# Optimization experiments

Measured on AMD Instinct MI355X. Metric: run time of the kernel, lower is better.

Reference implementation:

```python
import jax, jax.numpy as jnp
import numpy as np

N, E, D_IN, D_H, D_OUT = 50000, 800000, 128, 128, 40
EPS = 1e-5


def setup_inputs() -> dict:
    key = jax.random.key(0)
    ks = jax.random.split(key, 12)
    x = jax.random.normal(ks[0], (N, D_IN), dtype=jnp.float32)
    edge_index = jax.random.randint(ks[1], (2, E), 0, N, dtype=jnp.int32)
    s = 1.0 / np.sqrt(D_H)
    return {
        "x": x,
        "edge_index": edge_index,
        "W1": jax.random.normal(ks[2], (D_IN, D_H), jnp.float32) * s,
        "b1": jnp.zeros((D_H,), jnp.float32),
        "W2": jax.random.normal(ks[3], (D_H, D_H), jnp.float32) * s,
        "b2": jnp.zeros((D_H,), jnp.float32),
        "g1": jnp.ones((D_H,), jnp.float32),
        "be1": jnp.zeros((D_H,), jnp.float32),
        "g2": jnp.ones((D_H,), jnp.float32),
        "be2": jnp.zeros((D_H,), jnp.float32),
        "g3": jnp.ones((D_H,), jnp.float32),
        "be3": jnp.zeros((D_H,), jnp.float32),
        "Wm": jax.random.normal(ks[4], (D_H, D_OUT), jnp.float32) * s,
        "bm": jnp.zeros((D_OUT,), jnp.float32),
    }


def _gcn_conv(x, W, b, src, dst, dinv):
    # GCNConv: x' = D^{-1/2}(A+I)D^{-1/2} (x W) + b
    xw = x @ W                                   # [N, H]
    coef = dinv[src] * dinv[dst]                 # [E]
    agg = jax.ops.segment_sum(xw[src] * coef[:, None], dst, num_segments=x.shape[0])
    agg = agg + xw * (dinv * dinv)[:, None]      # self-loop term
    return agg + b


def _bn(x, g, b):
    # BatchNorm1d in training mode: biased batch statistics over nodes
    m = jnp.mean(x, axis=0)
    v = jnp.var(x, axis=0)
    return g * (x - m) * jax.lax.rsqrt(v + EPS) + b


def reference(x, edge_index, W1, b1, W2, b2, g1, be1, g2, be2, g3, be3, Wm, bm):
    src, dst = edge_index[0], edge_index[1]
    # degree with self-loops (GCN symmetric normalization, computed on dst/col)
    deg = 1.0 + jax.ops.segment_sum(jnp.ones((E,), jnp.float32), dst, num_segments=N)
    dinv = jax.lax.rsqrt(deg)
    h = _gcn_conv(x, W1, b1, src, dst, dinv)
    h = jax.nn.relu(_bn(h, g1, be1))            # dropout is identity in eval
    h = _gcn_conv(h, W2, b2, src, dst, dinv)
    h = jax.nn.relu(_bn(h, g2, be2))
    h = _bn(h, g3, be3)
    h = h @ Wm + bm
    return jax.nn.log_softmax(h, axis=1)
```

## Files before the change

### kernel.cpp

```cpp
#include <hip/hip_runtime.h>
#include <hip/hip_fp16.h>
#include <math.h>

#define BN_EPS 1e-5f
#define CAP 128
#define NSTAT 200

typedef __attribute__((ext_vector_type(8))) short short8;
typedef __attribute__((ext_vector_type(4))) float floatx4;

__device__ inline unsigned short f2bf(float f) {
    union { float f; unsigned u; } x; x.f = f;
    unsigned r = x.u + 0x7fff + ((x.u >> 16) & 1);
    return (unsigned short)(r >> 16);
}
__device__ inline float bf2f(unsigned short h) {
    union { float f; unsigned u; } x; x.u = ((unsigned)h) << 16; return x.f;
}
__device__ inline void bn_sc_sh(float sum, float sumsq, float g, float be, float invN,
                                float& sc, float& sh) {
    float mean = sum * invN;
    float var = sumsq * invN - mean * mean;
    sc = g * rsqrtf(var + BN_EPS);
    sh = be - mean * sc;
}

__device__ inline void pack_one(int idx, const float* W1, const float* W2, const float* Wm,
                                unsigned short* p1, unsigned short* p2, unsigned short* pm) {
    const float* W;
    unsigned short* pack;
    int f, l = idx & 63, t, n, stride, ncols;
    if (idx < 2048) {
        W = W1; pack = p1; f = idx >> 6; t = f >> 3; n = (f & 7) * 16 + (l & 15);
        stride = 128; ncols = 128;
    } else if (idx < 4096) {
        W = W2; pack = p2; f = (idx - 2048) >> 6; t = f >> 3; n = (f & 7) * 16 + (l & 15);
        stride = 128; ncols = 128;
    } else {
        W = Wm; pack = pm; f = (idx - 4096) >> 6; t = f / 3; n = (f % 3) * 16 + (l & 15);
        stride = 40; ncols = 40;
    }
    int q = l >> 4;
    unsigned short* pp = pack + f * 1024 + l * 16;
#pragma unroll
    for (int j = 0; j < 8; ++j) {
        int k = t * 32 + q * 8 + j;
        float v = (n < ncols) ? W[k * stride + n] : 0.f;
        unsigned short hi = f2bf(v);
        float lo = v - bf2f(hi);
        pp[j] = hi;
        pp[8 + j] = f2bf(lo);
    }
}

__global__ __launch_bounds__(256) void k_zero_pack(const float* W1, const float* W2,
                                                   const float* Wm, unsigned short* p1,
                                                   unsigned short* p2, unsigned short* pm,
                                                   int* fillc, float* stats, int N) {
    int gtid = blockIdx.x * 256 + threadIdx.x;
    int gsz = gridDim.x * 256;
    for (int i = gtid; i < N; i += gsz) fillc[i] = 0;
    for (int i = gtid; i < 768; i += gsz) stats[i] = 0.f;
    for (int i = gtid; i < 4864; i += gsz) pack_one(i, W1, W2, Wm, p1, p2, pm);
}

__global__ void k_fill(const int* __restrict__ src, const int* __restrict__ dst, int E,
                       int* __restrict__ fillc, unsigned short* __restrict__ col16) {
    int g = blockIdx.x & 7;
    int rank = blockIdx.x >> 3;
    int stride = (gridDim.x >> 3) * 256;
    for (int e = rank * 256 + threadIdx.x; e < E; e += stride) {
        int d = dst[e];
        if ((d & 7) != g) continue;
        int r = atomicAdd(&fillc[d], 1);
        if (r < CAP) col16[(size_t)d * CAP + r] = (unsigned short)src[e];
    }
}

__device__ inline void load_row8(const float* arow, int kbase, float av[8]) {
    float4 a0 = *(const float4*)(arow + kbase);
    float4 a1 = *(const float4*)(arow + kbase + 4);
    av[0] = a0.x; av[1] = a0.y; av[2] = a0.z; av[3] = a0.w;
    av[4] = a1.x; av[5] = a1.y; av[6] = a1.z; av[7] = a1.w;
}
__device__ inline void load_row8(const __half* arow, int kbase, float av[8]) {
    float4 raw = *(const float4*)(arow + kbase);
    const __half2* h = (const __half2*)&raw;
#pragma unroll
    for (int i = 0; i < 4; ++i) {
        float2 f = __half22float2(h[i]);
        av[2 * i] = f.x;
        av[2 * i + 1] = f.y;
    }
}

template <typename T, bool FUSE_BN>
__device__ void gemm_phase(const T* __restrict__ A, const unsigned short* __restrict__ packW,
                           const float* __restrict__ sums, const float* __restrict__ g,
                           const float* __restrict__ be, float invN,
                           const int* __restrict__ fillc, __half* __restrict__ C16, int M,
                           int waveId, int nwaves, int lane) {
    int row = lane & 15, quad = lane >> 4;
    for (int m0 = waveId * 16; m0 < M; m0 += nwaves * 16) {
        floatx4 acc[8];
#pragma unroll
        for (int nt = 0; nt < 8; ++nt) acc[nt] = (floatx4){0.f, 0.f, 0.f, 0.f};
        int mr = m0 + row;
        if (mr >= M) mr = M - 1;
        const T* arow = A + (size_t)mr * 128;
#pragma unroll
        for (int t = 0; t < 4; ++t) {
            int kbase = t * 32 + quad * 8;
            float av[8];
            load_row8(arow, kbase, av);
            if (FUSE_BN) {
#pragma unroll
                for (int j = 0; j < 8; ++j) {
                    int c = kbase + j;
                    float sc, sh;
                    bn_sc_sh(sums[c], sums[128 + c], g[c], be[c], invN, sc, sh);
                    av[j] = fmaxf(av[j] * sc + sh, 0.f);
                }
            }
            short8 ah, al;
#pragma unroll
            for (int j = 0; j < 8; ++j) {
                unsigned short hi = f2bf(av[j]);
                ah[j] = (short)hi;
                al[j] = (short)f2bf(av[j] - bf2f(hi));
            }
            const unsigned short* wp = packW + (size_t)(t * 8) * 1024 + lane * 16;
#pragma unroll
            for (int nt = 0; nt < 8; ++nt) {
                short8 wh = *(const short8*)wp;
                short8 wl = *(const short8*)(wp + 8);
                wp += 1024;
                acc[nt] = __builtin_amdgcn_mfma_f32_16x16x32_bf16(ah, wh, acc[nt], 0, 0, 0);
                acc[nt] = __builtin_amdgcn_mfma_f32_16x16x32_bf16(al, wh, acc[nt], 0, 0, 0);
                acc[nt] = __builtin_amdgcn_mfma_f32_16x16x32_bf16(ah, wl, acc[nt], 0, 0, 0);
            }
        }
        float d[4];
#pragma unroll
        for (int r = 0; r < 4; ++r) {
            int m = m0 + quad * 4 + r;
            d[r] = (m < M) ? rsqrtf(1.f + (float)fillc[m]) : 0.f;
        }
#pragma unroll
        for (int nt = 0; nt < 8; ++nt) {
#pragma unroll
            for (int r = 0; r < 4; ++r) {
                int m = m0 + quad * 4 + r;
                if (m < M)
                    C16[(size_t)m * 128 + nt * 16 + row] = __float2half_rn(acc[nt][r] * d[r]);
            }
        }
    }
}

__global__ __launch_bounds__(256) void k_gemm1(const float* A, const unsigned short* pW,
                                               const int* fillc, __half* C, int M) {
    gemm_phase<float, false>(A, pW, nullptr, nullptr, nullptr, 0.f, fillc, C, M,
                             blockIdx.x * 4 + (threadIdx.x >> 6), gridDim.x * 4,
                             threadIdx.x & 63);
}
__global__ __launch_bounds__(256) void k_gemm2(const __half* A, const unsigned short* pW,
                                               const float* sums, const float* g,
                                               const float* be, float invN, const int* fillc,
                                               __half* C, int M) {
    gemm_phase<__half, true>(A, pW, sums, g, be, invN, fillc, C, M,
                             blockIdx.x * 4 + (threadIdx.x >> 6), gridDim.x * 4,
                             threadIdx.x & 63);
}

__global__ __launch_bounds__(256) void k_gath(const __half* __restrict__ y16,
                                              const int* __restrict__ fillc,
                                              const unsigned short* __restrict__ col16,
                                              const float* __restrict__ bias,
                                              __half* __restrict__ out, int N) {
    int wv = threadIdx.x >> 6;
    int lane = threadIdx.x & 63;
    int n = blockIdx.x * 4 + wv;
    if (n >= N) return;
    int sub = lane >> 4;
    int c8 = (lane & 15) << 3;

    float acc[8];
#pragma unroll
    for (int i = 0; i < 8; ++i) acc[i] = 0.f;

    int degraw = fillc[n];
    int deg = min(degraw, CAP);
    const unsigned short* cb = col16 + (size_t)n * CAP;
    for (int jb = 0; jb < deg; jb += 64) {
        int cnt = min(64, deg - jb);
        int idx = (lane < cnt) ? (int)cb[jb + lane] : 0;
        int jj = 0;
        for (; jj + 16 <= cnt; jj += 16) {
            int s0 = __shfl(idx, jj + sub, 64);
            int s1 = __shfl(idx, jj + 4 + sub, 64);
            int s2 = __shfl(idx, jj + 8 + sub, 64);
            int s3 = __shfl(idx, jj + 12 + sub, 64);
            float4 r0 = *(const float4*)(y16 + (size_t)s0 * 128 + c8);
            float4 r1 = *(const float4*)(y16 + (size_t)s1 * 128 + c8);
            float4 r2 = *(const float4*)(y16 + (size_t)s2 * 128 + c8);
            float4 r3 = *(const float4*)(y16 + (size_t)s3 * 128 + c8);
            const __half2* h0 = (const __half2*)&r0;
            const __half2* h1 = (const __half2*)&r1;
            const __half2* h2 = (const __half2*)&r2;
            const __half2* h3 = (const __half2*)&r3;
#pragma unroll
            for (int i = 0; i < 4; ++i) {
                float2 f0 = __half22float2(h0[i]);
                float2 f1 = __half22float2(h1[i]);
                float2 f2 = __half22float2(h2[i]);
                float2 f3 = __half22float2(h3[i]);
                acc[2 * i] += (f0.x + f1.x) + (f2.x + f3.x);
                acc[2 * i + 1] += (f0.y + f1.y) + (f2.y + f3.y);
            }
        }
        for (; jj < cnt; jj += 4) {
            int jt = jj + sub;
            bool valid = jt < cnt;
            int s = __shfl(idx, valid ? jt : 0, 64);
            float4 r = *(const float4*)(y16 + (size_t)s * 128 + c8);
            if (valid) {
                const __half2* hh = (const __half2*)&r;
#pragma unroll
                for (int i = 0; i < 4; ++i) {
                    float2 f = __half22float2(hh[i]);
                    acc[2 * i] += f.x;
                    acc[2 * i + 1] += f.y;
                }
            }
        }
    }
#pragma unroll
    for (int i = 0; i < 8; ++i) {
        acc[i] += __shfl_xor(acc[i], 16, 64);
        acc[i] += __shfl_xor(acc[i], 32, 64);
    }
    if (sub == 0) {
        float dn = rsqrtf(1.f + (float)degraw);
        float4 selfraw = *(const float4*)(y16 + (size_t)n * 128 + c8);
        const __half2* sh = (const __half2*)&selfraw;
        float4 b0 = *(const float4*)(bias + c8);
        float4 b1 = *(const float4*)(bias + c8 + 4);
        float bb[8] = {b0.x, b0.y, b0.z, b0.w, b1.x, b1.y, b1.z, b1.w};
        __half2 o[4];
#pragma unroll
        for (int i = 0; i < 4; ++i) {
            float2 sf = __half22float2(sh[i]);
            float vx = dn * (acc[2 * i] + sf.x) + bb[2 * i];
            float vy = dn * (acc[2 * i + 1] + sf.y) + bb[2 * i + 1];
            o[i] = __float22half2_rn(make_float2(vx, vy));
        }
        *(float4*)(out + (size_t)n * 128 + c8) = *(float4*)o;
    }
}

template <bool TRANSFORM>
__global__ __launch_bounds__(256) void k_stats_s(const __half2* __restrict__ h, int N,
                                                 const float* __restrict__ sums2,
                                                 const float* __restrict__ g2,
                                                 const float* __restrict__ be2, float invN,
                                                 float* __restrict__ statsOut) {
    __shared__ float ls[4][256];
    int tid = threadIdx.x, bid = blockIdx.x;
    int cp = tid & 63, rg = tid >> 6;
    float scx = 1.f, shx = 0.f, scy = 1.f, shy = 0.f;
    if (TRANSFORM) {
        int c = cp * 2;
        bn_sc_sh(sums2[c], sums2[128 + c], g2[c], be2[c], invN, scx, shx);
        bn_sc_sh(sums2[c + 1], sums2[128 + c + 1], g2[c + 1], be2[c + 1], invN, scy, shy);
    }
    float sx = 0.f, sy = 0.f, s2x = 0.f, s2y = 0.f;
    for (int r = bid * 4 + rg; r < N; r += NSTAT * 4) {
        float2 v = __half22float2(h[(size_t)r * 64 + cp]);
        if (TRANSFORM) {
            v.x = fmaxf(v.x * scx + shx, 0.f);
            v.y = fmaxf(v.y * scy + shy, 0.f);
        }
        sx += v.x; sy += v.y;
        s2x += v.x * v.x; s2y += v.y * v.y;
    }
    ls[0][tid] = sx; ls[1][tid] = sy; ls[2][tid] = s2x; ls[3][tid] = s2y;
    __syncthreads();
    if (tid < 64) {
        float a0 = ls[0][tid] + ls[0][tid + 64] + ls[0][tid + 128] + ls[0][tid + 192];
        float a1 = ls[1][tid] + ls[1][tid + 64] + ls[1][tid + 128] + ls[1][tid + 192];
        float a2 = ls[2][tid] + ls[2][tid + 64] + ls[2][tid + 128] + ls[2][tid + 192];
        float a3 = ls[3][tid] + ls[3][tid + 64] + ls[3][tid + 128] + ls[3][tid + 192];
        atomicAdd(&statsOut[2 * tid], a0);
        atomicAdd(&statsOut[2 * tid + 1], a1);
        atomicAdd(&statsOut[128 + 2 * tid], a2);
        atomicAdd(&statsOut[128 + 2 * tid + 1], a3);
    }
}

__global__ __launch_bounds__(256) void k_final_s(const __half* __restrict__ h,
                                                 const float* __restrict__ sums2,
                                                 const float* __restrict__ g2,
                                                 const float* __restrict__ be2,
                                                 const float* __restrict__ sums3,
                                                 const float* __restrict__ g3,
                                                 const float* __restrict__ be3, float invN,
                                                 const unsigned short* __restrict__ packWm,
                                                 const float* __restrict__ bm,
                                                 float* __restrict__ out, int N) {
    int lane = threadIdx.x & 63;
    int wv = threadIdx.x >> 6;
    int m0 = (blockIdx.x * 4 + wv) * 16;
    if (m0 >= N) return;
    int row = lane & 15, quad = lane >> 4;

    floatx4 acc[3];
#pragma unroll
    for (int nt = 0; nt < 3; ++nt) acc[nt] = (floatx4){0.f, 0.f, 0.f, 0.f};

    int mr = m0 + row;
    if (mr >= N) mr = N - 1;
    const __half* arow = h + (size_t)mr * 128;
#pragma unroll
    for (int t = 0; t < 4; ++t) {
        int kbase = t * 32 + quad * 8;
        float av[8];
        load_row8(arow, kbase, av);
#pragma unroll
        for (int j = 0; j < 8; ++j) {
            int c = kbase + j;
            float sc2, sh2, sc3, sh3;
            bn_sc_sh(sums2[c], sums2[128 + c], g2[c], be2[c], invN, sc2, sh2);
            bn_sc_sh(sums3[c], sums3[128 + c], g3[c], be3[c], invN, sc3, sh3);
            av[j] = fmaxf(av[j] * sc2 + sh2, 0.f) * sc3 + sh3;
        }
        short8 ah, al;
#pragma unroll
        for (int j = 0; j < 8; ++j) {
            unsigned short hi = f2bf(av[j]);
            ah[j] = (short)hi;
            al[j] = (short)f2bf(av[j] - bf2f(hi));
        }
        const unsigned short* wp = packWm + (size_t)(t * 3) * 1024 + lane * 16;
#pragma unroll
        for (int nt = 0; nt < 3; ++nt) {
            short8 wh = *(const short8*)wp;
            short8 wl = *(const short8*)(wp + 8);
            wp += 1024;
            acc[nt] = __builtin_amdgcn_mfma_f32_16x16x32_bf16(ah, wh, acc[nt], 0, 0, 0);
            acc[nt] = __builtin_amdgcn_mfma_f32_16x16x32_bf16(al, wh, acc[nt], 0, 0, 0);
            acc[nt] = __builtin_amdgcn_mfma_f32_16x16x32_bf16(ah, wl, acc[nt], 0, 0, 0);
        }
    }
    float bb[3];
#pragma unroll
    for (int nt = 0; nt < 3; ++nt) {
        int col = nt * 16 + row;
        bb[nt] = (col < 40) ? bm[col] : 0.f;
    }
    bool val2 = (row < 8);
#pragma unroll
    for (int r = 0; r < 4; ++r) {
        int m = m0 + quad * 4 + r;
        float v0 = acc[0][r] + bb[0];
        float v1 = acc[1][r] + bb[1];
        float v2 = acc[2][r] + bb[2];
        float mx = fmaxf(v0, v1);
        if (val2) mx = fmaxf(mx, v2);
#pragma unroll
        for (int off = 1; off <= 8; off <<= 1) mx = fmaxf(mx, __shfl_xor(mx, off, 64));
        float s = expf(v0 - mx) + expf(v1 - mx) + (val2 ? expf(v2 - mx) : 0.f);
#pragma unroll
        for (int off = 1; off <= 8; off <<= 1) s += __shfl_xor(s, off, 64);
        float lse = mx + logf(s);
        if (m < N) {
            out[(size_t)m * 40 + row] = v0 - lse;
            out[(size_t)m * 40 + 16 + row] = v1 - lse;
            if (val2) out[(size_t)m * 40 + 32 + row] = v2 - lse;
        }
    }
}

extern "C" void kernel_launch(void* const* d_in, const int* in_sizes, int n_in,
                              void* d_out, int out_size, void* d_ws, size_t ws_size,
                              hipStream_t stream) {
    const float* x   = (const float*)d_in[0];
    const int*   ei  = (const int*)d_in[1];
    const float* W1  = (const float*)d_in[2];
    const float* b1  = (const float*)d_in[3];
    const float* W2  = (const float*)d_in[4];
    const float* b2  = (const float*)d_in[5];
    const float* g1  = (const float*)d_in[6];
    const float* be1 = (const float*)d_in[7];
    const float* g2  = (const float*)d_in[8];
    const float* be2 = (const float*)d_in[9];
    const float* g3  = (const float*)d_in[10];
    const float* be3 = (const float*)d_in[11];
    const float* Wm  = (const float*)d_in[12];
    const float* bm  = (const float*)d_in[13];
    float* out = (float*)d_out;

    int N = in_sizes[0] / 128;
    int E = in_sizes[1] / 2;
    float invN = 1.0f / (float)N;

    char* ws = (char*)d_ws;
    size_t off = 0;
    auto alloc = [&](size_t bytes) -> void* {
        void* p = ws + off;
        off += (bytes + 255) & ~(size_t)255;
        return p;
    };
    int*   fillc    = (int*)alloc((size_t)N * 4);
    float* statsAll = (float*)alloc(768 * 4);
    unsigned short* col16 = (unsigned short*)alloc((size_t)N * CAP * 2);
    unsigned short* pW1 = (unsigned short*)alloc(32768 * 2);
    unsigned short* pW2 = (unsigned short*)alloc(32768 * 2);
    unsigned short* pWm = (unsigned short*)alloc(12288 * 2);
    __half* y16 = (__half*)alloc((size_t)N * 128 * 2);
    __half* h16 = (__half*)alloc((size_t)N * 128 * 2);
    (void)ws_size; (void)n_in; (void)out_size;

    int gb = (N + 63) / 64;
    int gatherb = (N + 3) / 4;

    k_zero_pack<<<64, 256, 0, stream>>>(W1, W2, Wm, pW1, pW2, pWm, fillc, statsAll, N);
    k_fill<<<1024, 256, 0, stream>>>(ei, ei + E, E, fillc, col16);

    k_gemm1<<<gb, 256, 0, stream>>>(x, pW1, fillc, y16, N);
    k_gath<<<gatherb, 256, 0, stream>>>(y16, fillc, col16, b1, h16, N);
    k_stats_s<false><<<NSTAT, 256, 0, stream>>>((const __half2*)h16, N, nullptr, nullptr,
                                                nullptr, invN, statsAll);
    k_gemm2<<<gb, 256, 0, stream>>>(h16, pW2, statsAll, g1, be1, invN, fillc, y16, N);
    k_gath<<<gatherb, 256, 0, stream>>>(y16, fillc, col16, b2, h16, N);
    k_stats_s<false><<<NSTAT, 256, 0, stream>>>((const __half2*)h16, N, nullptr, nullptr,
                                                nullptr, invN, statsAll + 256);
    k_stats_s<true><<<NSTAT, 256, 0, stream>>>((const __half2*)h16, N, statsAll + 256, g2, be2,
                                               invN, statsAll + 512);
    k_final_s<<<gb, 256, 0, stream>>>(h16, statsAll + 256, g2, be2, statsAll + 512, g3, be3,
                                      invN, pWm, bm, out, N);
}
```

Measured before the change: 340.7 us.

## Merge pipeline stages into cooperative persistent kernels with grid syncs

Replaces the chain of separate launches (zero/pack, fill, gather, stats, final) with three cooperative persistent kernels that use grid.sync between phases, keeping the two GEMMs as normal launches. The aim is to remove per-kernel launch gaps and tail effects across the many small stages. In exchange, gathers now use a grid-stride loop over a fixed grid, which may reduce latency hiding, and each grid sync has its own cost. A fallback to the old launch sequence remains for when cooperative launch fails.

```diff
diff --git a/kernel.cpp b/kernel.cpp
--- a/kernel.cpp
+++ b/kernel.cpp
@@ -1,6 +1,9 @@
 #include <hip/hip_runtime.h>
 #include <hip/hip_fp16.h>
+#include <hip/hip_cooperative_groups.h>
 #include <math.h>
+
+namespace cg = cooperative_groups;
 
 #define BN_EPS 1e-5f
 #define CAP 128
@@ -53,30 +56,6 @@
     }
 }
 
-__global__ __launch_bounds__(256) void k_zero_pack(const float* W1, const float* W2,
-                                                   const float* Wm, unsigned short* p1,
-                                                   unsigned short* p2, unsigned short* pm,
-                                                   int* fillc, float* stats, int N) {
-    int gtid = blockIdx.x * 256 + threadIdx.x;
-    int gsz = gridDim.x * 256;
-    for (int i = gtid; i < N; i += gsz) fillc[i] = 0;
-    for (int i = gtid; i < 768; i += gsz) stats[i] = 0.f;
-    for (int i = gtid; i < 4864; i += gsz) pack_one(i, W1, W2, Wm, p1, p2, pm);
-}
-
-__global__ void k_fill(const int* __restrict__ src, const int* __restrict__ dst, int E,
-                       int* __restrict__ fillc, unsigned short* __restrict__ col16) {
-    int g = blockIdx.x & 7;
-    int rank = blockIdx.x >> 3;
-    int stride = (gridDim.x >> 3) * 256;
-    for (int e = rank * 256 + threadIdx.x; e < E; e += stride) {
-        int d = dst[e];
-        if ((d & 7) != g) continue;
-        int r = atomicAdd(&fillc[d], 1);
-        if (r < CAP) col16[(size_t)d * CAP + r] = (unsigned short)src[e];
-    }
-}
-
 __device__ inline void load_row8(const float* arow, int kbase, float av[8]) {
     float4 a0 = *(const float4*)(arow + kbase);
     float4 a1 = *(const float4*)(arow + kbase + 4);
@@ -173,120 +152,115 @@
                              threadIdx.x & 63);
 }
 
-__global__ __launch_bounds__(256) void k_gath(const __half* __restrict__ y16,
-                                              const int* __restrict__ fillc,
-                                              const unsigned short* __restrict__ col16,
-                                              const float* __restrict__ bias,
-                                              __half* __restrict__ out, int N) {
-    int wv = threadIdx.x >> 6;
-    int lane = threadIdx.x & 63;
-    int n = blockIdx.x * 4 + wv;
-    if (n >= N) return;
+__device__ void gather_phase16(const __half* __restrict__ y16, const int* __restrict__ fillc,
+                               const unsigned short* __restrict__ col16,
+                               const float* __restrict__ bias, __half* __restrict__ out, int N,
+                               int waveId, int nwaves, int lane) {
     int sub = lane >> 4;
     int c8 = (lane & 15) << 3;
-
-    float acc[8];
-#pragma unroll
-    for (int i = 0; i < 8; ++i) acc[i] = 0.f;
-
-    int degraw = fillc[n];
-    int deg = min(degraw, CAP);
-    const unsigned short* cb = col16 + (size_t)n * CAP;
-    for (int jb = 0; jb < deg; jb += 64) {
-        int cnt = min(64, deg - jb);
-        int idx = (lane < cnt) ? (int)cb[jb + lane] : 0;
-        int jj = 0;
-        for (; jj + 16 <= cnt; jj += 16) {
-            int s0 = __shfl(idx, jj + sub, 64);
-            int s1 = __shfl(idx, jj + 4 + sub, 64);
-            int s2 = __shfl(idx, jj + 8 + sub, 64);
-            int s3 = __shfl(idx, jj + 12 + sub, 64);
-            float4 r0 = *(const float4*)(y16 + (size_t)s0 * 128 + c8);
-            float4 r1 = *(const float4*)(y16 + (size_t)s1 * 128 + c8);
-            float4 r2 = *(const float4*)(y16 + (size_t)s2 * 128 + c8);
-            float4 r3 = *(const float4*)(y16 + (size_t)s3 * 128 + c8);
-            const __half2* h0 = (const __half2*)&r0;
-            const __half2* h1 = (const __half2*)&r1;
-            const __half2* h2 = (const __half2*)&r2;
-            const __half2* h3 = (const __half2*)&r3;
+    for (int n = waveId; n < N; n += nwaves) {
+        float acc[8];
+#pragma unroll
+        for (int i = 0; i < 8; ++i) acc[i] = 0.f;
+        int degraw = fillc[n];
+        int deg = min(degraw, CAP);
+        const unsigned short* cb = col16 + (size_t)n * CAP;
+        for (int jb = 0; jb < deg; jb += 64) {
+            int cnt = min(64, deg - jb);
+            int idx = (lane < cnt) ? (int)cb[jb + lane] : 0;
+            int jj = 0;
+            for (; jj + 16 <= cnt; jj += 16) {
+                int s0 = __shfl(idx, jj + sub, 64);
+                int s1 = __shfl(idx, jj + 4 + sub, 64);
+                int s2 = __shfl(idx, jj + 8 + sub, 64);
+                int s3 = __shfl(idx, jj + 12 + sub, 64);
+                float4 r0 = *(const float4*)(y16 + (size_t)s0 * 128 + c8);
+                float4 r1 = *(const float4*)(y16 + (size_t)s1 * 128 + c8);
+                float4 r2 = *(const float4*)(y16 + (size_t)s2 * 128 + c8);
+                float4 r3 = *(const float4*)(y16 + (size_t)s3 * 128 + c8);
+                const __half2* h0 = (const __half2*)&r0;
+                const __half2* h1 = (const __half2*)&r1;
+                const __half2* h2 = (const __half2*)&r2;
+                const __half2* h3 = (const __half2*)&r3;
+#pragma unroll
+                for (int i = 0; i < 4; ++i) {
+                    float2 f0 = __half22float2(h0[i]);
+                    float2 f1 = __half22float2(h1[i]);
+                    float2 f2 = __half22float2(h2[i]);
+                    float2 f3 = __half22float2(h3[i]);
+                    acc[2 * i] += (f0.x + f1.x) + (f2.x + f3.x);
+                    acc[2 * i + 1] += (f0.y + f1.y) + (f2.y + f3.y);
+                }
+            }
+            for (; jj < cnt; jj += 4) {
+                int jt = jj + sub;
+                bool valid = jt < cnt;
+                int s = __shfl(idx, valid ? jt : 0, 64);
+                float4 r = *(const float4*)(y16 + (size_t)s * 128 + c8);
+                if (valid) {
+                    const __half2* hh = (const __half2*)&r;
+#pragma unroll
+                    for (int i = 0; i < 4; ++i) {
+                        float2 f = __half22float2(hh[i]);
+                        acc[2 * i] += f.x;
+                        acc[2 * i + 1] += f.y;
+                    }
+                }
+            }
+        }
+#pragma unroll
+        for (int i = 0; i < 8; ++i) {
+            acc[i] += __shfl_xor(acc[i], 16, 64);
+            acc[i] += __shfl_xor(acc[i], 32, 64);
+        }
+        if (sub == 0) {
+            float dn = rsqrtf(1.f + (float)degraw);
+            float4 selfraw = *(const float4*)(y16 + (size_t)n * 128 + c8);
+            const __half2* sh = (const __half2*)&selfraw;
+            float4 b0 = *(const float4*)(bias + c8);
+            float4 b1 = *(const float4*)(bias + c8 + 4);
+            float bb[8] = {b0.x, b0.y, b0.z, b0.w, b1.x, b1.y, b1.z, b1.w};
+            __half2 o[4];
 #pragma unroll
             for (int i = 0; i < 4; ++i) {
-                float2 f0 = __half22float2(h0[i]);
-                float2 f1 = __half22float2(h1[i]);
-                float2 f2 = __half22float2(h2[i]);
-                float2 f3 = __half22float2(h3[i]);
-                acc[2 * i] += (f0.x + f1.x) + (f2.x + f3.x);
-                acc[2 * i + 1] += (f0.y + f1.y) + (f2.y + f3.y);
-            }
-        }
-        for (; jj < cnt; jj += 4) {
-            int jt = jj + sub;
-            bool valid = jt < cnt;
-            int s = __shfl(idx, valid ? jt : 0, 64);
-            float4 r = *(const float4*)(y16 + (size_t)s * 128 + c8);
-            if (valid) {
-                const __half2* hh = (const __half2*)&r;
-#pragma unroll
-                for (int i = 0; i < 4; ++i) {
-                    float2 f = __half22float2(hh[i]);
-                    acc[2 * i] += f.x;
-                    acc[2 * i + 1] += f.y;
-                }
-            }
-        }
-    }
-#pragma unroll
-    for (int i = 0; i < 8; ++i) {
-        acc[i] += __shfl_xor(acc[i], 16, 64);
-        acc[i] += __shfl_xor(acc[i], 32, 64);
-    }
-    if (sub == 0) {
-        float dn = rsqrtf(1.f + (float)degraw);
-        float4 selfraw = *(const float4*)(y16 + (size_t)n * 128 + c8);
-        const __half2* sh = (const __half2*)&selfraw;
-        float4 b0 = *(const float4*)(bias + c8);
-        float4 b1 = *(const float4*)(bias + c8 + 4);
-        float bb[8] = {b0.x, b0.y, b0.z, b0.w, b1.x, b1.y, b1.z, b1.w};
-        __half2 o[4];
-#pragma unroll
-        for (int i = 0; i < 4; ++i) {
-            float2 sf = __half22float2(sh[i]);
-            float vx = dn * (acc[2 * i] + sf.x) + bb[2 * i];
-            float vy = dn * (acc[2 * i + 1] + sf.y) + bb[2 * i + 1];
-            o[i] = __float22half2_rn(make_float2(vx, vy));
-        }
-        *(float4*)(out + (size_t)n * 128 + c8) = *(float4*)o;
+                float2 sf = __half22float2(sh[i]);
+                float vx = dn * (acc[2 * i] + sf.x) + bb[2 * i];
+                float vy = dn * (acc[2 * i + 1] + sf.y) + bb[2 * i + 1];
+                o[i] = __float22half2_rn(make_float2(vx, vy));
+            }
+            *(float4*)(out + (size_t)n * 128 + c8) = *(float4*)o;
+        }
     }
 }
 
 template <bool TRANSFORM>
-__global__ __launch_bounds__(256) void k_stats_s(const __half2* __restrict__ h, int N,
-                                                 const float* __restrict__ sums2,
-                                                 const float* __restrict__ g2,
-                                                 const float* __restrict__ be2, float invN,
-                                                 float* __restrict__ statsOut) {
-    __shared__ float ls[4][256];
-    int tid = threadIdx.x, bid = blockIdx.x;
+__device__ void stats_phase(const __half2* __restrict__ h, int N,
+                            const float* __restrict__ sums2, const float* __restrict__ g2,
+                            const float* __restrict__ be2, float invN,
+                            float* __restrict__ statsOut, int tid, int bid, float (*ls)[256]) {
     int cp = tid & 63, rg = tid >> 6;
-    float scx = 1.f, shx = 0.f, scy = 1.f, shy = 0.f;
-    if (TRANSFORM) {
-        int c = cp * 2;
-        bn_sc_sh(sums2[c], sums2[128 + c], g2[c], be2[c], invN, scx, shx);
-        bn_sc_sh(sums2[c + 1], sums2[128 + c + 1], g2[c + 1], be2[c + 1], invN, scy, shy);
-    }
     float sx = 0.f, sy = 0.f, s2x = 0.f, s2y = 0.f;
-    for (int r = bid * 4 + rg; r < N; r += NSTAT * 4) {
-        float2 v = __half22float2(h[(size_t)r * 64 + cp]);
+    if (bid < NSTAT) {
+        float scx = 1.f, shx = 0.f, scy = 1.f, shy = 0.f;
         if (TRANSFORM) {
-            v.x = fmaxf(v.x * scx + shx, 0.f);
-            v.y = fmaxf(v.y * scy + shy, 0.f);
-        }
-        sx += v.x; sy += v.y;
-        s2x += v.x * v.x; s2y += v.y * v.y;
-    }
+            int c = cp * 2;
+            bn_sc_sh(sums2[c], sums2[128 + c], g2[c], be2[c], invN, scx, shx);
+            bn_sc_sh(sums2[c + 1], sums2[128 + c + 1], g2[c + 1], be2[c + 1], invN, scy, shy);
+        }
+        for (int r = bid * 4 + rg; r < N; r += NSTAT * 4) {
+            float2 v = __half22float2(h[(size_t)r * 64 + cp]);
+            if (TRANSFORM) {
+                v.x = fmaxf(v.x * scx + shx, 0.f);
+                v.y = fmaxf(v.y * scy + shy, 0.f);
+            }
+            sx += v.x; sy += v.y;
+            s2x += v.x * v.x; s2y += v.y * v.y;
+        }
+    }
+    __syncthreads();
     ls[0][tid] = sx; ls[1][tid] = sy; ls[2][tid] = s2x; ls[3][tid] = s2y;
     __syncthreads();
-    if (tid < 64) {
+    if (bid < NSTAT && tid < 64) {
         float a0 = ls[0][tid] + ls[0][tid + 64] + ls[0][tid + 128] + ls[0][tid + 192];
         float a1 = ls[1][tid] + ls[1][tid + 64] + ls[1][tid + 128] + ls[1][tid + 192];
         float a2 = ls[2][tid] + ls[2][tid + 64] + ls[2][tid + 128] + ls[2][tid + 192];
@@ -296,89 +270,202 @@
         atomicAdd(&statsOut[128 + 2 * tid], a2);
         atomicAdd(&statsOut[128 + 2 * tid + 1], a3);
     }
-}
-
-__global__ __launch_bounds__(256) void k_final_s(const __half* __restrict__ h,
-                                                 const float* __restrict__ sums2,
-                                                 const float* __restrict__ g2,
-                                                 const float* __restrict__ be2,
-                                                 const float* __restrict__ sums3,
-                                                 const float* __restrict__ g3,
-                                                 const float* __restrict__ be3, float invN,
-                                                 const unsigned short* __restrict__ packWm,
-                                                 const float* __restrict__ bm,
-                                                 float* __restrict__ out, int N) {
+    __syncthreads();
+}
+
+__device__ void final_phase(const __half* __restrict__ h, const float* __restrict__ sums2,
+                            const float* __restrict__ g2, const float* __restrict__ be2,
+                            const float* __restrict__ sums3, const float* __restrict__ g3,
+                            const float* __restrict__ be3, float invN,
+                            const unsigned short* __restrict__ packWm,
+                            const float* __restrict__ bm, float* __restrict__ out, int N,
+                            int waveId, int nwaves, int lane) {
+    int row = lane & 15, quad = lane >> 4;
+    int units = (N + 15) >> 4;
+    for (int u = waveId; u < units; u += nwaves) {
+        int m0 = u << 4;
+        floatx4 acc[3];
+#pragma unroll
+        for (int nt = 0; nt < 3; ++nt) acc[nt] = (floatx4){0.f, 0.f, 0.f, 0.f};
+        int mr = m0 + row;
+        if (mr >= N) mr = N - 1;
+        const __half* arow = h + (size_t)mr * 128;
+#pragma unroll
+        for (int t = 0; t < 4; ++t) {
+            int kbase = t * 32 + quad * 8;
+            float av[8];
+            load_row8(arow, kbase, av);
+#pragma unroll
+            for (int j = 0; j < 8; ++j) {
+                int c = kbase + j;
+                float sc2, sh2, sc3, sh3;
+                bn_sc_sh(sums2[c], sums2[128 + c], g2[c], be2[c], invN, sc2, sh2);
+                bn_sc_sh(sums3[c], sums3[128 + c], g3[c], be3[c], invN, sc3, sh3);
+                av[j] = fmaxf(av[j] * sc2 + sh2, 0.f) * sc3 + sh3;
+            }
+            short8 ah, al;
+#pragma unroll
+            for (int j = 0; j < 8; ++j) {
+                unsigned short hi = f2bf(av[j]);
+                ah[j] = (short)hi;
+                al[j] = (short)f2bf(av[j] - bf2f(hi));
+            }
+            const unsigned short* wp = packWm + (size_t)(t * 3) * 1024 + lane * 16;
+#pragma unroll
+            for (int nt = 0; nt < 3; ++nt) {
+                short8 wh = *(const short8*)wp;
+                short8 wl = *(const short8*)(wp + 8);
+                wp += 1024;
+                acc[nt] = __builtin_amdgcn_mfma_f32_16x16x32_bf16(ah, wh, acc[nt], 0, 0, 0);
+                acc[nt] = __builtin_amdgcn_mfma_f32_16x16x32_bf16(al, wh, acc[nt], 0, 0, 0);
+                acc[nt] = __builtin_amdgcn_mfma_f32_16x16x32_bf16(ah, wl, acc[nt], 0, 0, 0);
+            }
+        }
+        float bb[3];
+#pragma unroll
+        for (int nt = 0; nt < 3; ++nt) {
+            int col = nt * 16 + row;
+            bb[nt] = (col < 40) ? bm[col] : 0.f;
+        }
+        bool val2 = (row < 8);
+#pragma unroll
+        for (int r = 0; r < 4; ++r) {
+            int m = m0 + quad * 4 + r;
+            float v0 = acc[0][r] + bb[0];
+            float v1 = acc[1][r] + bb[1];
+            float v2 = acc[2][r] + bb[2];
+            float mx = fmaxf(v0, v1);
+            if (val2) mx = fmaxf(mx, v2);
+#pragma unroll
+            for (int off = 1; off <= 8; off <<= 1) mx = fmaxf(mx, __shfl_xor(mx, off, 64));
+            float s = expf(v0 - mx) + expf(v1 - mx) + (val2 ? expf(v2 - mx) : 0.f);
+#pragma unroll
+            for (int off = 1; off <= 8; off <<= 1) s += __shfl_xor(s, off, 64);
+            float lse = mx + logf(s);
+            if (m < N) {
+                out[(size_t)m * 40 + row] = v0 - lse;
+                out[(size_t)m * 40 + 16 + row] = v1 - lse;
+                if (val2) out[(size_t)m * 40 + 32 + row] = v2 - lse;
+            }
+        }
+    }
+}
+
+struct PrepP {
+    const int* ei; int E; int N;
+    const float* W1; const float* W2; const float* Wm;
+    unsigned short* p1; unsigned short* p2; unsigned short* pm;
+    int* fillc; float* stats; unsigned short* col16;
+};
+__global__ __launch_bounds__(256) void k_phaseA(PrepP p) {
+    cg::grid_group grid = cg::this_grid();
+    int gtid = blockIdx.x * 256 + threadIdx.x, gsz = gridDim.x * 256;
+    for (int i = gtid; i < p.N; i += gsz) p.fillc[i] = 0;
+    for (int i = gtid; i < 768; i += gsz) p.stats[i] = 0.f;
+    for (int i = gtid; i < 4864; i += gsz) pack_one(i, p.W1, p.W2, p.Wm, p.p1, p.p2, p.pm);
+    __threadfence();
+    grid.sync();
+    const int* srcs = p.ei;
+    const int* dsts = p.ei + p.E;
+    int g = blockIdx.x & 7;
+    int rank = blockIdx.x >> 3;
+    int stride = (gridDim.x >> 3) * 256;
+    for (int e = rank * 256 + threadIdx.x; e < p.E; e += stride) {
+        int d = dsts[e];
+        if ((d & 7) != g) continue;
+        int r = atomicAdd(&p.fillc[d], 1);
+        if (r < CAP) p.col16[(size_t)d * CAP + r] = (unsigned short)srcs[e];
+    }
+}
+
+struct L1P {
+    const __half* y16; const int* fillc; const unsigned short* col16;
+    const float* b1; __half* h16; float* stats1; int N; float invN;
+};
+__global__ __launch_bounds__(256) void k_phaseB(L1P p) {
+    cg::grid_group grid = cg::this_grid();
+    __shared__ float ls[4][256];
     int lane = threadIdx.x & 63;
-    int wv = threadIdx.x >> 6;
-    int m0 = (blockIdx.x * 4 + wv) * 16;
-    if (m0 >= N) return;
-    int row = lane & 15, quad = lane >> 4;
-
-    floatx4 acc[3];
-#pragma unroll
-    for (int nt = 0; nt < 3; ++nt) acc[nt] = (floatx4){0.f, 0.f, 0.f, 0.f};
-
-    int mr = m0 + row;
-    if (mr >= N) mr = N - 1;
-    const __half* arow = h + (size_t)mr * 128;
-#pragma unroll
-    for (int t = 0; t < 4; ++t) {
-        int kbase = t * 32 + quad * 8;
-        float av[8];
-        load_row8(arow, kbase, av);
-#pragma unroll
-        for (int j = 0; j < 8; ++j) {
-            int c = kbase + j;
-            float sc2, sh2, sc3, sh3;
-            bn_sc_sh(sums2[c], sums2[128 + c], g2[c], be2[c], invN, sc2, sh2);
-            bn_sc_sh(sums3[c], sums3[128 + c], g3[c], be3[c], invN, sc3, sh3);
-            av[j] = fmaxf(av[j] * sc2 + sh2, 0.f) * sc3 + sh3;
-        }
-        short8 ah, al;
-#pragma unroll
-        for (int j = 0; j < 8; ++j) {
-            unsigned short hi = f2bf(av[j]);
-            ah[j] = (short)hi;
-            al[j] = (short)f2bf(av[j] - bf2f(hi));
-        }
-        const unsigned short* wp = packWm + (size_t)(t * 3) * 1024 + lane * 16;
-#pragma unroll
-        for (int nt = 0; nt < 3; ++nt) {
-            short8 wh = *(const short8*)wp;
-            short8 wl = *(const short8*)(wp + 8);
-            wp += 1024;
-            acc[nt] = __builtin_amdgcn_mfma_f32_16x16x32_bf16(ah, wh, acc[nt], 0, 0, 0);
-            acc[nt] = __builtin_amdgcn_mfma_f32_16x16x32_bf16(al, wh, acc[nt], 0, 0, 0);
-            acc[nt] = __builtin_amdgcn_mfma_f32_16x16x32_bf16(ah, wl, acc[nt], 0, 0, 0);
-        }
-    }
-    float bb[3];
-#pragma unroll
-    for (int nt = 0; nt < 3; ++nt) {
-        int col = nt * 16 + row;
-        bb[nt] = (col < 40) ? bm[col] : 0.f;
-    }
-    bool val2 = (row < 8);
-#pragma unroll
-    for (int r = 0; r < 4; ++r) {
-        int m = m0 + quad * 4 + r;
-        float v0 = acc[0][r] + bb[0];
-        float v1 = acc[1][r] + bb[1];
-        float v2 = acc[2][r] + bb[2];
-        float mx = fmaxf(v0, v1);
-        if (val2) mx = fmaxf(mx, v2);
-#pragma unroll
-        for (int off = 1; off <= 8; off <<= 1) mx = fmaxf(mx, __shfl_xor(mx, off, 64));
-        float s = expf(v0 - mx) + expf(v1 - mx) + (val2 ? expf(v2 - mx) : 0.f);
-#pragma unroll
-        for (int off = 1; off <= 8; off <<= 1) s += __shfl_xor(s, off, 64);
-        float lse = mx + logf(s);
-        if (m < N) {
-            out[(size_t)m * 40 + row] = v0 - lse;
-            out[(size_t)m * 40 + 16 + row] = v1 - lse;
-            if (val2) out[(size_t)m * 40 + 32 + row] = v2 - lse;
-        }
-    }
+    int waveId = blockIdx.x * 4 + (threadIdx.x >> 6);
+    int nwaves = gridDim.x * 4;
+    gather_phase16(p.y16, p.fillc, p.col16, p.b1, p.h16, p.N, waveId, nwaves, lane);
+    __threadfence();
+    grid.sync();
+    stats_phase<false>((const __half2*)p.h16, p.N, nullptr, nullptr, nullptr, p.invN, p.stats1,
+                       threadIdx.x, blockIdx.x, ls);
+}
+
+struct L2P {
+    const __half* y16; const int* fillc; const unsigned short* col16;
+    const float* b2; __half* h16;
+    float* stats2; float* stats3;
+    const float* g2; const float* be2; const float* g3; const float* be3;
+    const unsigned short* pWm; const float* bm; float* out;
+    int N; float invN;
+};
+__global__ __launch_bounds__(256) void k_phaseC(L2P p) {
+    cg::grid_group grid = cg::this_grid();
+    __shared__ float ls[4][256];
+    int lane = threadIdx.x & 63;
+    int waveId = blockIdx.x * 4 + (threadIdx.x >> 6);
+    int nwaves = gridDim.x * 4;
+    gather_phase16(p.y16, p.fillc, p.col16, p.b2, p.h16, p.N, waveId, nwaves, lane);
+    __threadfence();
+    grid.sync();
+    stats_phase<false>((const __half2*)p.h16, p.N, nullptr, nullptr, nullptr, p.invN, p.stats2,
+                       threadIdx.x, blockIdx.x, ls);
+    __threadfence();
+    grid.sync();
+    stats_phase<true>((const __half2*)p.h16, p.N, p.stats2, p.g2, p.be2, p.invN, p.stats3,
+                      threadIdx.x, blockIdx.x, ls);
+    __threadfence();
+    grid.sync();
+    final_phase(p.h16, p.stats2, p.g2, p.be2, p.stats3, p.g3, p.be3, p.invN, p.pWm, p.bm,
+                p.out, p.N, waveId, nwaves, lane);
+}
+
+__global__ __launch_bounds__(256) void k_zero_pack(const float* W1, const float* W2,
+                                                   const float* Wm, unsigned short* p1,
+                                                   unsigned short* p2, unsigned short* pm,
+                                                   int* fillc, float* stats, int N) {
+    int gtid = blockIdx.x * 256 + threadIdx.x, gsz = gridDim.x * 256;
+    for (int i = gtid; i < N; i += gsz) fillc[i] = 0;
+    for (int i = gtid; i < 768; i += gsz) stats[i] = 0.f;
+    for (int i = gtid; i < 4864; i += gsz) pack_one(i, W1, W2, Wm, p1, p2, pm);
+}
+__global__ void k_fill(const int* src, const int* dst, int E, int* fillc,
+                       unsigned short* col16) {
+    int g = blockIdx.x & 7;
+    int rank = blockIdx.x >> 3;
+    int stride = (gridDim.x >> 3) * 256;
+    for (int e = rank * 256 + threadIdx.x; e < E; e += stride) {
+        int d = dst[e];
+        if ((d & 7) != g) continue;
+        int r = atomicAdd(&fillc[d], 1);
+        if (r < CAP) col16[(size_t)d * CAP + r] = (unsigned short)src[e];
+    }
+}
+__global__ __launch_bounds__(256) void k_gath(const __half* y16, const int* fillc,
+                                              const unsigned short* col16, const float* bias,
+                                              __half* out, int N) {
+    gather_phase16(y16, fillc, col16, bias, out, N, blockIdx.x * 4 + (threadIdx.x >> 6),
+                   gridDim.x * 4, threadIdx.x & 63);
+}
+template <bool TR>
+__global__ __launch_bounds__(256) void k_stats_s(const __half2* h, int N, const float* sums2,
+                                                 const float* g2, const float* be2, float invN,
+                                                 float* statsOut) {
+    __shared__ float ls[4][256];
+    stats_phase<TR>(h, N, sums2, g2, be2, invN, statsOut, threadIdx.x, blockIdx.x, ls);
+}
+__global__ __launch_bounds__(256) void k_final_s(const __half* h, const float* sums2,
+                                                 const float* g2, const float* be2,
+                                                 const float* sums3, const float* g3,
+                                                 const float* be3, float invN,
+                                                 const unsigned short* pWm, const float* bm,
+                                                 float* out, int N) {
+    final_phase(h, sums2, g2, be2, sums3, g3, be3, invN, pWm, bm, out, N,
+                blockIdx.x * 4 + (threadIdx.x >> 6), gridDim.x * 4, threadIdx.x & 63);
 }
 
 extern "C" void kernel_launch(void* const* d_in, const int* in_sizes, int n_in,
@@ -422,11 +509,44 @@
     (void)ws_size; (void)n_in; (void)out_size;
 
     int gb = (N + 63) / 64;
+
+    PrepP pa = {ei, E, N, W1, W2, Wm, pW1, pW2, pWm, fillc, statsAll, col16};
+    L1P pb = {y16, fillc, col16, b1, h16, statsAll, N, invN};
+    L2P pc = {y16,  fillc, col16, b2, h16, statsAll + 256, statsAll + 512,
+              g2,   be2,   g3,    be3, pWm, bm,            out,
+              N,    invN};
+
+    int mbA = 0, mbB = 0, mbC = 0;
+    bool ok = true;
+    ok &= hipOccupancyMaxActiveBlocksPerMultiprocessor(&mbA, k_phaseA, 256, 0) == hipSuccess;
+    ok &= hipOccupancyMaxActiveBlocksPerMultiprocessor(&mbB, k_phaseB, 256, 0) == hipSuccess;
+    ok &= hipOccupancyMaxActiveBlocksPerMultiprocessor(&mbC, k_phaseC, 256, 0) == hipSuccess;
+    ok = ok && mbA >= 1 && mbB >= 1 && mbC >= 1;
+
+    if (ok) {
+        int gA = ((mbA > 8 ? 8 : mbA) * 256) & ~7;
+        int gB = (mbB > 8 ? 8 : mbB) * 256;
+        int gC = (mbC > 8 ? 8 : mbC) * 256;
+        void* aA[] = {&pa};
+        void* aB[] = {&pb};
+        void* aC[] = {&pc};
+        hipError_t e1 =
+            hipLaunchCooperativeKernel((void*)k_phaseA, dim3(gA), dim3(256), aA, 0, stream);
+        if (e1 == hipSuccess) {
+            k_gemm1<<<gb, 256, 0, stream>>>(x, pW1, fillc, y16, N);
+            hipError_t e2 = hipLaunchCooperativeKernel((void*)k_phaseB, dim3(gB), dim3(256),
+                                                       aB, 0, stream);
+            k_gemm2<<<gb, 256, 0, stream>>>(h16, pW2, statsAll, g1, be1, invN, fillc, y16, N);
+            hipError_t e3 = hipLaunchCooperativeKernel((void*)k_phaseC, dim3(gC), dim3(256),
+                                                       aC, 0, stream);
+            if (e2 == hipSuccess && e3 == hipSuccess) return;
+        }
+        ok = false;
+    }
+
     int gatherb = (N + 3) / 4;
-
     k_zero_pack<<<64, 256, 0, stream>>>(W1, W2, Wm, pW1, pW2, pWm, fillc, statsAll, N);
     k_fill<<<1024, 256, 0, stream>>>(ei, ei + E, E, fillc, col16);
-
     k_gemm1<<<gb, 256, 0, stream>>>(x, pW1, fillc, y16, N);
     k_gath<<<gatherb, 256, 0, stream>>>(y16, fillc, col16, b1, h16, N);
     k_stats_s<false><<<NSTAT, 256, 0, stream>>>((const __half2*)h16, N, nullptr, nullptr,
```

New measurement: 371.3 us. 1.09x slower.
